# Kernel optimization log

Measured on AMD Instinct MI355X. Metric: run time of the kernel, lower is better.

## Reference

```python
import jax, jax.numpy as jnp
import numpy as np

EPS = 1.1920929e-07  # torch RMSNorm default eps = finfo(fp32).eps


def _rmsnorm(x, w):
    return x * jax.lax.rsqrt(jnp.mean(x * x, axis=-1, keepdims=True) + EPS) * w


def setup_inputs() -> dict:
    B, S, D, H, SD = 2, 2048, 1024, 16, 64
    ks = jax.random.split(jax.random.key(0), 16)
    scale = 0.02
    return {
        "x": jax.random.normal(ks[0], (B, S, D), jnp.float32),
        "gamma": jax.random.normal(ks[1], (1, 1, D), jnp.float32),
        "beta": jax.random.normal(ks[2], (1, 1, D), jnp.float32),
        "state": jax.random.normal(ks[3], (B, SD), jnp.float32),
        # weights stored as (in, out) so y = x @ W
        "w_qkv": jax.random.normal(ks[4], (D, 3 * D), jnp.float32) * scale,
        "w_o": jax.random.normal(ks[5], (D, D), jnp.float32) * scale,
        "w_gate": jax.random.normal(ks[6], (D, 3 * D), jnp.float32) * scale,
        "w_up": jax.random.normal(ks[7], (D, 3 * D), jnp.float32) * scale,
        "w_down": jax.random.normal(ks[8], (3 * D, D), jnp.float32) * scale,
        "norm1_w": jnp.ones((D,), jnp.float32),
        "norm2_w": jnp.ones((D,), jnp.float32),
        "w_state_mod": jax.random.normal(ks[9], (SD, 2 * D), jnp.float32) * scale,
        "w_h2s": jax.random.normal(ks[10], (D, SD), jnp.float32) * scale,
        "w_sgate": jax.random.normal(ks[11], (2 * SD, SD), jnp.float32) * scale,
    }


def reference(x, gamma, beta, state, w_qkv, w_o, w_gate, w_up, w_down,
              norm1_w, norm2_w, w_state_mod, w_h2s, w_sgate):
    B, S, D = x.shape
    H = 16
    hd = D // H

    # state-conditioned FiLM modulation
    state_mod = state @ w_state_mod                      # (B, 2D)
    state_gamma = 1.0 + state_mod[:, :D][:, None, :]     # (B, 1, D)
    state_beta = state_mod[:, D:][:, None, :]
    full_gamma = gamma * state_gamma
    full_beta = beta + state_beta

    # attention branch
    h = _rmsnorm(x, norm1_w) * full_gamma + full_beta
    qkv = (h @ w_qkv).reshape(B, S, 3, H, hd)
    q = qkv[:, :, 0].transpose(0, 2, 1, 3)               # (B, H, S, hd)
    k = qkv[:, :, 1].transpose(0, 2, 1, 3)
    v = qkv[:, :, 2].transpose(0, 2, 1, 3)
    scores = jnp.einsum('bhqd,bhkd->bhqk', q, k) / np.sqrt(hd).astype(np.float32)
    causal = jnp.tril(jnp.ones((S, S), bool))
    scores = jnp.where(causal, scores, -jnp.inf)
    attn = jax.nn.softmax(scores, axis=-1)
    out = jnp.einsum('bhqk,bhkd->bhqd', attn, v).transpose(0, 2, 1, 3).reshape(B, S, D)
    x = x + out @ w_o

    # SwiGLU FFN branch (same FiLM params)
    h2 = _rmsnorm(x, norm2_w) * full_gamma + full_beta
    gate = jax.nn.silu(h2 @ w_gate)
    x = x + (gate * (h2 @ w_up)) @ w_down

    # recurrent state update
    new_info = jnp.mean(x, axis=1) @ w_h2s               # (B, SD)
    update_gate = jax.nn.sigmoid(jnp.concatenate([state, new_info], axis=-1) @ w_sgate)
    new_state = state * (1.0 - update_gate) + new_info * update_gate
    return x, new_state
```

## Files before the change

kernel.cpp:

```cpp
#include <hip/hip_runtime.h>
#include <hip/hip_bf16.h>

#define EPS_RMS 1.1920929e-07f

constexpr int B_ = 2, S_ = 2048, D_ = 1024, H_ = 16, HD_ = 64, SD_ = 64;
constexpr int M_ = B_ * S_;
constexpr int D3_ = 3 * D_;

using short8 = __attribute__((ext_vector_type(8))) short;
using f32x4  = __attribute__((ext_vector_type(4))) float;
using f32x16 = __attribute__((ext_vector_type(16))) float;
typedef int v2i __attribute__((ext_vector_type(2)));

static __device__ __forceinline__ ushort f2bf(float x) {
  __hip_bfloat16 h = __float2bfloat16(x);
  return *reinterpret_cast<ushort*>(&h);
}
static __device__ __forceinline__ float bf2f(ushort u) {
  __hip_bfloat16 h;
  *reinterpret_cast<ushort*>(&h) = u;
  return __bfloat162float(h);
}
static __device__ __forceinline__ unsigned pk2(float lo, float hi) {
  return (unsigned)f2bf(lo) | ((unsigned)f2bf(hi) << 16);
}
static __device__ __forceinline__ v2i swap32(int a, int b) {
  return __builtin_amdgcn_permlane32_swap(a, b, false, false);
}
struct alignas(8) bf4 { ushort a, b, c, d; };

static __device__ __forceinline__ void gload16(const ushort* g, ushort* l) {
  __builtin_amdgcn_global_load_lds(
      (const __attribute__((address_space(1))) unsigned int*)g,
      (__attribute__((address_space(3))) unsigned int*)l, 16, 0, 0);
}

__global__ void film_kernel(const float* __restrict__ state,
                            const float* __restrict__ w_sm,
                            const float* __restrict__ gamma,
                            const float* __restrict__ beta,
                            float* __restrict__ fg, float* __restrict__ fb) {
  int c = blockIdx.x * 256 + threadIdx.x;
  int b = blockIdx.y;
  float acc = 0.f;
#pragma unroll 8
  for (int k = 0; k < SD_; ++k)
    acc += state[b * SD_ + k] * w_sm[k * (2 * D_) + c];
  if (c < D_) fg[b * D_ + c] = gamma[c] * (1.f + acc);
  else        fb[b * D_ + (c - D_)] = beta[c - D_] + acc;
}

__global__ __launch_bounds__(256) void rmsnorm_film_kernel(
    const float* __restrict__ X, const float* __restrict__ nw,
    const float* __restrict__ fg, const float* __restrict__ fb,
    ushort* __restrict__ Hout) {
  int row = blockIdx.x;
  int b = row / S_;
  int t = threadIdx.x;
  const float4* x4 = (const float4*)(X + (size_t)row * D_);
  float4 xv = x4[t];
  float ss = xv.x * xv.x + xv.y * xv.y + xv.z * xv.z + xv.w * xv.w;
#pragma unroll
  for (int off = 32; off >= 1; off >>= 1) ss += __shfl_xor(ss, off);
  __shared__ float red[4];
  if ((t & 63) == 0) red[t >> 6] = ss;
  __syncthreads();
  float tot = red[0] + red[1] + red[2] + red[3];
  float scale = rsqrtf(tot / (float)D_ + EPS_RMS);
  int d = t * 4;
  const float4 nw4 = *(const float4*)(nw + d);
  const float4 g4  = *(const float4*)(fg + b * D_ + d);
  const float4 b4  = *(const float4*)(fb + b * D_ + d);
  bf4 hv;
  hv.a = f2bf(xv.x * scale * nw4.x * g4.x + b4.x);
  hv.b = f2bf(xv.y * scale * nw4.y * g4.y + b4.y);
  hv.c = f2bf(xv.z * scale * nw4.z * g4.z + b4.z);
  hv.d = f2bf(xv.w * scale * nw4.w * g4.w + b4.w);
  *(bf4*)(Hout + (size_t)row * D_ + d) = hv;
}

__global__ __launch_bounds__(256) void transpose_bf16(
    const float* __restrict__ W, ushort* __restrict__ Wt, int K, int N) {
  __shared__ float tile[32][33];
  int n0 = blockIdx.x * 32, k0 = blockIdx.y * 32;
  int t = threadIdx.x;
  int c = t & 31, r = t >> 5;
#pragma unroll
  for (int p = 0; p < 4; ++p)
    tile[r + 8 * p][c] = W[(size_t)(k0 + r + 8 * p) * N + n0 + c];
  __syncthreads();
#pragma unroll
  for (int p = 0; p < 4; ++p)
    Wt[(size_t)(n0 + r + 8 * p) * K + k0 + c] = f2bf(tile[c][r + 8 * p]);
}

__global__ __launch_bounds__(256) void transpose_bf16_dual(
    const float* __restrict__ W0, ushort* __restrict__ T0,
    const float* __restrict__ W1, ushort* __restrict__ T1, int K, int N) {
  const float* W = blockIdx.z ? W1 : W0;
  ushort* Wt = blockIdx.z ? T1 : T0;
  __shared__ float tile[32][33];
  int n0 = blockIdx.x * 32, k0 = blockIdx.y * 32;
  int t = threadIdx.x;
  int c = t & 31, r = t >> 5;
#pragma unroll
  for (int p = 0; p < 4; ++p)
    tile[r + 8 * p][c] = W[(size_t)(k0 + r + 8 * p) * N + n0 + c];
  __syncthreads();
#pragma unroll
  for (int p = 0; p < 4; ++p)
    Wt[(size_t)(n0 + r + 8 * p) * K + k0 + c] = f2bf(tile[c][r + 8 * p]);
}

static __device__ __forceinline__ void mfma_tile(
    const char* Au, const char* Bu, f32x4 (&acc)[4][4],
    int l15, int l4, int swz, int wr, int wc) {
#pragma unroll
  for (int kk = 0; kk < 2; ++kk) {
    int tslot = ((kk * 4 + l4) ^ swz) << 4;
    short8 a[4], b[4];
#pragma unroll
    for (int i = 0; i < 4; ++i) {
      int arow = wr * 64 + i * 16 + l15;
      int brow = wc * 64 + i * 16 + l15;
      a[i] = *(const short8*)(Au + arow * 128 + tslot);
      b[i] = *(const short8*)(Bu + brow * 128 + tslot);
    }
#pragma unroll
    for (int m = 0; m < 4; ++m)
#pragma unroll
      for (int n = 0; n < 4; ++n)
        acc[m][n] = __builtin_amdgcn_mfma_f32_16x16x32_bf16(a[m], b[n], acc[m][n], 0, 0, 0);
  }
}

static __device__ __forceinline__ void block_swizzle(int bid, int M, int N,
                                                     int& bm, int& bn) {
  int nbn = N >> 7;
  int nb  = nbn * (M >> 7);
  int qx  = nb >> 3;
  int lin = (bid & 7) * qx + (bid >> 3);
  int grp = lin / (nbn << 3), rem = lin % (nbn << 3);
  bm = ((grp << 3) + (rem & 7)) << 7;
  bn = (rem >> 3) << 7;
}

template<int EPI>
__global__ __launch_bounds__(256, 3) void gemm_mfma(
    const ushort* __restrict__ A, const ushort* __restrict__ Bt,
    const float* __restrict__ Res,
    float* __restrict__ Cf, ushort* __restrict__ Cb, ushort* __restrict__ VtP,
    int M, int N, int K) {
  __shared__ ushort smem[16384];
  char* Au = (char*)smem;
  char* Bu = (char*)(smem + 8192);
  int t = threadIdx.x;
  int bm, bn;
  block_swizzle(blockIdx.x, M, N, bm, bn);

  int lane = t & 63, wid = t >> 6;
  int wr = wid >> 1, wc = wid & 1;
  int l15 = lane & 15, l4 = lane >> 4;
  int swz = l15 & 7;

  const ushort* gA[4];
  const ushort* gB[4];
  ushort* lA[4];
  ushort* lB[4];
#pragma unroll
  for (int p = 0; p < 4; ++p) {
    int seg = p * 4 + wid;
    int flat = seg * 64 + lane;
    int row = flat >> 3, sl = flat & 7;
    int gc = ((sl ^ (row & 7)) << 3);
    gA[p] = A  + (size_t)(bm + row) * K + gc;
    gB[p] = Bt + (size_t)(bn + row) * K + gc;
    lA[p] = smem + seg * 512;
    lB[p] = smem + 8192 + seg * 512;
  }

  f32x4 acc[4][4];
#pragma unroll
  for (int m = 0; m < 4; ++m)
#pragma unroll
    for (int n = 0; n < 4; ++n) acc[m][n] = (f32x4){0.f, 0.f, 0.f, 0.f};

  int nk = K >> 6;
  for (int kt = 0; kt < nk; ++kt) {
    __syncthreads();
#pragma unroll
    for (int p = 0; p < 4; ++p) {
      gload16(gA[p], lA[p]);
      gload16(gB[p], lB[p]);
      gA[p] += 64; gB[p] += 64;
    }
    __syncthreads();
    mfma_tile(Au, Bu, acc, l15, l4, swz, wr, wc);
  }

  if constexpr (EPI == 3) {
#pragma unroll
    for (int m = 0; m < 4; ++m)
#pragma unroll
      for (int n = 0; n < 4; ++n) {
        int row0 = bm + wr * 64 + m * 16 + l4 * 4;
        int col  = bn + wc * 64 + n * 16 + l15;
#pragma unroll
        for (int j = 0; j < 4; ++j) {
          size_t idx = (size_t)(row0 + j) * (size_t)N + col;
          Cf[idx] = Res[idx] + acc[m][n][j];
        }
      }
  } else {
    __syncthreads();
    ushort* Es = smem;
    bool vblk = (bn >= 2048);
#pragma unroll
    for (int m = 0; m < 4; ++m)
#pragma unroll
      for (int n = 0; n < 4; ++n) {
        int rb0 = wr * 64 + m * 16 + l4 * 4;
        int c   = wc * 64 + n * 16 + l15;
#pragma unroll
        for (int j = 0; j < 4; ++j) {
          float v = acc[m][n][j];
          int r = rb0 + j;
          if (vblk) Es[c * 128 + (r ^ ((c & 15) << 3))] = f2bf(v);
          else      Es[r * 128 + c] = f2bf(v);
        }
      }
    __syncthreads();
    if (vblk) {
#pragma unroll
      for (int p = 0; p < 8; ++p) {
        int flat = p * 256 + t;
        int c = flat >> 4, r8 = (flat & 15) * 8;
        int vc = bn - 2048 + c, hh = vc >> 6, dd = vc & 63;
        int bbv = bm >> 11, s0 = (bm & 2047) + r8;
        *(short8*)(VtP + ((((size_t)bbv * 16 + hh) * 64 + dd) << 11) + s0) =
            *(const short8*)&Es[c * 128 + (r8 ^ ((c & 15) << 3))];
      }
    } else {
#pragma unroll
      for (int p = 0; p < 8; ++p) {
        int flat = p * 256 + t;
        int r = flat >> 4, c8 = (flat & 15) * 8;
        *(short8*)(Cb + (size_t)(bm + r) * N + bn + c8) = *(const short8*)&Es[r * 128 + c8];
      }
    }
  }
}

__global__ __launch_bounds__(256, 2) void gemm_dual(
    const ushort* __restrict__ A, const ushort* __restrict__ Gt,
    const ushort* __restrict__ Ut, ushort* __restrict__ Cb,
    int M, int N, int K) {
  __shared__ ushort smem[24576];
  char* Au = (char*)smem;
  char* Gu = (char*)(smem + 8192);
  char* Uu = (char*)(smem + 16384);
  int t = threadIdx.x;
  int bm, bn;
  block_swizzle(blockIdx.x, M, N, bm, bn);

  int lane = t & 63, wid = t >> 6;
  int wr = wid >> 1, wc = wid & 1;
  int l15 = lane & 15, l4 = lane >> 4;
  int swz = l15 & 7;

  const ushort* gA[4]; const ushort* gG[4]; const ushort* gU[4];
  ushort* lA[4]; ushort* lG[4]; ushort* lU[4];
#pragma unroll
  for (int p = 0; p < 4; ++p) {
    int seg = p * 4 + wid;
    int flat = seg * 64 + lane;
    int row = flat >> 3, sl = flat & 7;
    int gc = ((sl ^ (row & 7)) << 3);
    gA[p] = A  + (size_t)(bm + row) * K + gc;
    gG[p] = Gt + (size_t)(bn + row) * K + gc;
    gU[p] = Ut + (size_t)(bn + row) * K + gc;
    lA[p] = smem + seg * 512;
    lG[p] = smem + 8192 + seg * 512;
    lU[p] = smem + 16384 + seg * 512;
  }

  f32x4 ag[4][4], au[4][4];
#pragma unroll
  for (int m = 0; m < 4; ++m)
#pragma unroll
    for (int n = 0; n < 4; ++n) {
      ag[m][n] = (f32x4){0.f, 0.f, 0.f, 0.f};
      au[m][n] = (f32x4){0.f, 0.f, 0.f, 0.f};
    }

  int nk = K >> 6;
  for (int kt = 0; kt < nk; ++kt) {
    __syncthreads();
#pragma unroll
    for (int p = 0; p < 4; ++p) {
      gload16(gA[p], lA[p]);
      gload16(gG[p], lG[p]);
      gload16(gU[p], lU[p]);
      gA[p] += 64; gG[p] += 64; gU[p] += 64;
    }
    __syncthreads();
#pragma unroll
    for (int kk = 0; kk < 2; ++kk) {
      int tslot = ((kk * 4 + l4) ^ swz) << 4;
      short8 a[4], bg[4], bu[4];
#pragma unroll
      for (int i = 0; i < 4; ++i) {
        int arow = wr * 64 + i * 16 + l15;
        int brow = wc * 64 + i * 16 + l15;
        a[i]  = *(const short8*)(Au + arow * 128 + tslot);
        bg[i] = *(const short8*)(Gu + brow * 128 + tslot);
        bu[i] = *(const short8*)(Uu + brow * 128 + tslot);
      }
#pragma unroll
      for (int m = 0; m < 4; ++m)
#pragma unroll
        for (int n = 0; n < 4; ++n) {
          ag[m][n] = __builtin_amdgcn_mfma_f32_16x16x32_bf16(a[m], bg[n], ag[m][n], 0, 0, 0);
          au[m][n] = __builtin_amdgcn_mfma_f32_16x16x32_bf16(a[m], bu[n], au[m][n], 0, 0, 0);
        }
    }
  }

  __syncthreads();
  ushort* Es = smem;
#pragma unroll
  for (int m = 0; m < 4; ++m)
#pragma unroll
    for (int n = 0; n < 4; ++n) {
      int rb0 = wr * 64 + m * 16 + l4 * 4;
      int c   = wc * 64 + n * 16 + l15;
#pragma unroll
      for (int j = 0; j < 4; ++j) {
        float gv = ag[m][n][j];
        float v = gv / (1.f + __expf(-gv)) * au[m][n][j];
        Es[(rb0 + j) * 128 + c] = f2bf(v);
      }
    }
  __syncthreads();
#pragma unroll
  for (int p = 0; p < 8; ++p) {
    int flat = p * 256 + t;
    int r = flat >> 4, c8 = (flat & 15) * 8;
    *(short8*)(Cb + (size_t)(bm + r) * N + bn + c8) = *(const short8*)&Es[r * 128 + c8];
  }
}

__global__ __launch_bounds__(512, 2) void attn_mfma_kernel(
    const ushort* __restrict__ qkv,
    const ushort* __restrict__ Vt,
    ushort* __restrict__ AO) {
  __shared__ ushort lds[16384];
  const float SL2 = 0.125f * 1.44269504f;
  int t = threadIdx.x;
  int x = blockIdx.x;
  int lin = ((x & 7) << 5) + (x >> 3);
  int pp = lin & 7;
  int hb = lin >> 3;
  int h = hb & 15, bb = hb >> 4;
  int lane = t & 63, wv = t >> 6;
  int qi = wv >> 2, wsub = wv & 3;
  int qt = qi ? (15 - pp) : pp;
  int q0 = qt * 128;
  int l31 = lane & 31, g = lane >> 5;

  int qrow = q0 + wsub * 32 + l31;
  const ushort* qrow_ptr = qkv + (size_t)(bb * S_ + qrow) * 3072 + h * 64;
  short8 qf[4];
#pragma unroll
  for (int s = 0; s < 4; ++s) qf[s] = *(const short8*)(qrow_ptr + s * 16 + g * 8);

  f32x16 accO[2];
#pragma unroll
  for (int u = 0; u < 2; ++u)
#pragma unroll
    for (int r = 0; r < 16; ++r) accO[u][r] = 0.f;
  float m = -INFINITY, l = 0.f;
  int qg = qrow;
  int qmin = q0 + wsub * 32, qmax = qmin + 31;
  int nt = 2 * (16 - pp);

  const ushort* kbase = qkv + (size_t)(bb * S_) * 3072 + 1024 + h * 64;
  const ushort* vbase = Vt + ((size_t)(bb * 16 + h) * 64) * 2048;

  int srow = t >> 3, sslot = t & 7;
  int soff = srow * 64 + ((sslot ^ (srow & 7)) << 3);
  const ushort* kg0 = kbase + (size_t)srow * 3072 + sslot * 8;
  const ushort* vg0 = vbase + (size_t)srow * 2048 + sslot * 8;

  *(short8*)&lds[soff] = *(const short8*)kg0;
  *(short8*)&lds[4096 + soff] = *(const short8*)vg0;
  __syncthreads();

  for (int kti = 0; kti < nt; ++kti) {
    int cur = kti & 1;
    int kt = kti << 6;
    bool pf = (kti + 1 < nt);
    short8 rk, rv;
    if (pf) {
      rk = *(const short8*)(kg0 + (size_t)(kti + 1) * (64 * 3072));
      rv = *(const short8*)(vg0 + (kti + 1) * 64);
    }
    if (kt <= qmax) {
      const ushort* Kb = lds + cur * 8192;
      const ushort* Vb = Kb + 4096;

      f32x16 accT[2];
#pragma unroll
      for (int t2 = 0; t2 < 2; ++t2)
#pragma unroll
        for (int r = 0; r < 16; ++r) accT[t2][r] = 0.f;
      __builtin_amdgcn_s_setprio(1);
#pragma unroll
      for (int t2 = 0; t2 < 2; ++t2) {
        int key = 32 * t2 + l31;
#pragma unroll
        for (int s = 0; s < 4; ++s) {
          short8 kf = *(const short8*)&Kb[key * 64 + (((2 * s + g) ^ (key & 7)) << 3)];
          accT[t2] = __builtin_amdgcn_mfma_f32_32x32x16_bf16(kf, qf[s], accT[t2], 0, 0, 0);
        }
      }
      __builtin_amdgcn_s_setprio(0);

      bool need_mask = (kt + 63 > qmin);
      float p_[2][16];
      float pmax = -INFINITY;
#pragma unroll
      for (int t2 = 0; t2 < 2; ++t2)
#pragma unroll
        for (int r = 0; r < 16; ++r) {
          float v = accT[t2][r] * SL2;
          if (need_mask) {
            int key = kt + 32 * t2 + (r & 3) + 8 * (r >> 2) + 4 * g;
            if (key > qg) v = -INFINITY;
          }
          p_[t2][r] = v;
          pmax = fmaxf(pmax, v);
        }
      {
        v2i pm = swap32(__float_as_int(pmax), __float_as_int(pmax));
        pmax = fmaxf(pmax, __int_as_float(g ? pm.x : pm.y));
      }

      if (__any(pmax > m + 11.5f)) {
        float mnew = fmaxf(m, pmax);
        float corr = exp2f(m - mnew);
        m = mnew;
        l *= corr;
        float cr[16];
#pragma unroll
        for (int r = 0; r < 16; ++r) cr[r] = __shfl(corr, (r & 3) + 8 * (r >> 2) + 4 * g);
#pragma unroll
        for (int r = 0; r < 16; ++r) { accO[0][r] *= cr[r]; accO[1][r] *= cr[r]; }
      }
      float psum = 0.f;
#pragma unroll
      for (int t2 = 0; t2 < 2; ++t2)
#pragma unroll
        for (int r = 0; r < 16; ++r) {
          float e = exp2f(p_[t2][r] - m);
          p_[t2][r] = e;
          psum += e;
        }
      {
        v2i ps = swap32(__float_as_int(psum), __float_as_int(psum));
        psum += __int_as_float(g ? ps.x : ps.y);
      }
      l += psum;

#pragma unroll
      for (int s = 0; s < 4; ++s) {
        int ca = 2 * s, cb2 = 2 * s + 1;
        int ta = ca >> 2, ra = (ca & 3) * 4;
        int tb = cb2 >> 2, rbq = (cb2 & 3) * 4;
        int w0a = (int)pk2(p_[ta][ra], p_[ta][ra + 1]);
        int w1a = (int)pk2(p_[ta][ra + 2], p_[ta][ra + 3]);
        int w0b = (int)pk2(p_[tb][rbq], p_[tb][rbq + 1]);
        int w1b = (int)pk2(p_[tb][rbq + 2], p_[tb][rbq + 3]);
        v2i r0 = swap32(w0a, w0b);
        v2i r1 = swap32(w1a, w1b);
        union { int u[4]; short8 s8; } pa;
        pa.u[0] = r0.x;
        pa.u[1] = r1.x;
        pa.u[2] = r0.y;
        pa.u[3] = r1.y;
        __builtin_amdgcn_s_setprio(1);
#pragma unroll
        for (int u = 0; u < 2; ++u) {
          int d = 32 * u + l31;
          short8 vf = *(const short8*)&Vb[d * 64 + (((2 * s + g) ^ (d & 7)) << 3)];
          accO[u] = __builtin_amdgcn_mfma_f32_32x32x16_bf16(pa.s8, vf, accO[u], 0, 0, 0);
        }
        __builtin_amdgcn_s_setprio(0);
      }
    }
    if (pf) {
      ushort* dst = lds + (cur ^ 1) * 8192;
      *(short8*)&dst[soff] = rk;
      *(short8*)&dst[4096 + soff] = rv;
    }
    __syncthreads();
  }

  float linv = 1.f / l;
  float lr[16];
#pragma unroll
  for (int r = 0; r < 16; ++r) lr[r] = __shfl(linv, (r & 3) + 8 * (r >> 2) + 4 * g);
#pragma unroll
  for (int r = 0; r < 16; ++r) {
    int row = wv * 32 + (r & 3) + 8 * (r >> 2) + 4 * g;
    lds[row * 64 + l31]      = f2bf(accO[0][r] * lr[r]);
    lds[row * 64 + 32 + l31] = f2bf(accO[1][r] * lr[r]);
  }
  __syncthreads();
#pragma unroll
  for (int p = 0; p < 4; ++p) {
    int flat = p * 512 + t;
    int row = flat >> 3, slot = flat & 7;
    int qto = (row < 128) ? pp : (15 - pp);
    int grow = row & 127;
    *(short8*)(AO + (size_t)(bb * S_ + qto * 128 + grow) * 1024 + h * 64 + slot * 8) =
        *(const short8*)&lds[row * 64 + slot * 8];
  }
}

__global__ void colmean1(const float* __restrict__ X, float* __restrict__ part) {
  int d = blockIdx.x * 256 + threadIdx.x;
  int b = blockIdx.y;
  int ch = blockIdx.z;
  float s = 0.f;
  int s0 = ch * (S_ / 16);
  for (int i = 0; i < S_ / 16; ++i)
    s += X[(size_t)(b * S_ + s0 + i) * D_ + d];
  part[(b * 16 + ch) * D_ + d] = s;
}
__global__ void colmean2(const float* __restrict__ part, float* __restrict__ cm) {
  int d = blockIdx.x * 256 + threadIdx.x;
  int b = blockIdx.y;
  float s = 0.f;
#pragma unroll
  for (int c = 0; c < 16; ++c) s += part[(b * 16 + c) * D_ + d];
  cm[b * D_ + d] = s * (1.f / (float)S_);
}

__global__ __launch_bounds__(128) void state_kernel(
    const float* __restrict__ cm, const float* __restrict__ state,
    const float* __restrict__ w_h2s, const float* __restrict__ w_sg,
    float* __restrict__ out_tail) {
  int t = threadIdx.x;
  int b = t >> 6, j = t & 63;
  float ni = 0.f;
  for (int k = 0; k < D_; ++k) ni += cm[b * D_ + k] * w_h2s[k * SD_ + j];
  __shared__ float ni_s[128];
  ni_s[t] = ni;
  __syncthreads();
  float g = 0.f;
#pragma unroll
  for (int k = 0; k < SD_; ++k) g += state[b * SD_ + k] * w_sg[k * SD_ + j];
#pragma unroll
  for (int k = 0; k < SD_; ++k) g += ni_s[b * SD_ + k] * w_sg[(SD_ + k) * SD_ + j];
  g = 1.f / (1.f + __expf(-g));
  float st = state[b * SD_ + j];
  out_tail[b * SD_ + j] = st * (1.f - g) + ni * g;
}

extern "C" void kernel_launch(void* const* d_in, const int* in_sizes, int n_in,
                              void* d_out, int out_size, void* d_ws, size_t ws_size,
                              hipStream_t stream) {
  const float* x      = (const float*)d_in[0];
  const float* gamma  = (const float*)d_in[1];
  const float* beta   = (const float*)d_in[2];
  const float* state  = (const float*)d_in[3];
  const float* w_qkv  = (const float*)d_in[4];
  const float* w_o    = (const float*)d_in[5];
  const float* w_gate = (const float*)d_in[6];
  const float* w_up   = (const float*)d_in[7];
  const float* w_down = (const float*)d_in[8];
  const float* norm1w = (const float*)d_in[9];
  const float* norm2w = (const float*)d_in[10];
  const float* w_sm   = (const float*)d_in[11];
  const float* w_h2s  = (const float*)d_in[12];
  const float* w_sg   = (const float*)d_in[13];
  float* out = (float*)d_out;

  float* ws = (float*)d_ws;
  float*  fg     = ws;
  float*  fb     = ws + 2048;
  float*  cm     = ws + 4096;
  float*  part   = ws + 8192;
  ushort* h_bf   = (ushort*)(ws + 65536);
  ushort* AO_bf  = (ushort*)(ws + 65536 + 2097152);
  ushort* wT     = (ushort*)(ws + 65536 + 2 * 2097152);
  ushort* wT2    = (ushort*)(ws + 65536 + 2 * 2097152 + 1572864);
  ushort* qkv_bf = (ushort*)(ws + 65536 + 2 * 2097152 + 2 * 1572864);
  ushort* Vt_g   = (ushort*)(ws + 65536 + 2 * 2097152 + 2 * 1572864 + 6291456);
  ushort* gu_bf  = qkv_bf;

  film_kernel<<<dim3(8, B_), 256, 0, stream>>>(state, w_sm, gamma, beta, fg, fb);
  rmsnorm_film_kernel<<<M_, 256, 0, stream>>>(x, norm1w, fg, fb, h_bf);
  transpose_bf16<<<dim3(D3_ / 32, D_ / 32), 256, 0, stream>>>(w_qkv, wT, D_, D3_);
  gemm_mfma<4><<<(D3_ / 128) * (M_ / 128), 256, 0, stream>>>(
      h_bf, wT, nullptr, nullptr, qkv_bf, Vt_g, M_, D3_, D_);
  attn_mfma_kernel<<<256, 512, 0, stream>>>(qkv_bf, Vt_g, AO_bf);
  transpose_bf16<<<dim3(D_ / 32, D_ / 32), 256, 0, stream>>>(w_o, wT, D_, D_);
  gemm_mfma<3><<<(D_ / 128) * (M_ / 128), 256, 0, stream>>>(
      AO_bf, wT, x, out, nullptr, nullptr, M_, D_, D_);
  rmsnorm_film_kernel<<<M_, 256, 0, stream>>>(out, norm2w, fg, fb, h_bf);
  transpose_bf16_dual<<<dim3(D3_ / 32, D_ / 32, 2), 256, 0, stream>>>(
      w_gate, wT, w_up, wT2, D_, D3_);
  gemm_dual<<<(D3_ / 128) * (M_ / 128), 256, 0, stream>>>(
      h_bf, wT, wT2, gu_bf, M_, D3_, D_);
  transpose_bf16<<<dim3(D_ / 32, D3_ / 32), 256, 0, stream>>>(w_down, wT, D3_, D_);
  gemm_mfma<3><<<(D_ / 128) * (M_ / 128), 256, 0, stream>>>(
      gu_bf, wT, out, out, nullptr, nullptr, M_, D_, D3_);
  colmean1<<<dim3(4, B_, 16), 256, 0, stream>>>(out, part);
  colmean2<<<dim3(4, B_), 256, 0, stream>>>(part, cm);
  state_kernel<<<1, 128, 0, stream>>>(cm, state, w_h2s, w_sg, out + (size_t)M_ * D_);
}
```

Measured before the change: 317.3 us.

## Split attention blocks into one query tile each, longest-first scheduling

The attention kernel previously paired a short and a long causal query tile in one 512-thread block to balance work. It now launches 512 blocks of 256 threads, each handling a single 128-row query tile, ordered so the heaviest tiles are dispatched first, and K/V staging now uses two loads per thread. Launch bounds are adjusted for higher occupancy, and gemm_dual also gets a higher occupancy hint. This trades the paired-tile balancing for finer-grained blocks and dynamic scheduling, which may help latency hiding but loses K/V tile sharing across the two query tiles.

```diff
diff --git a/kernel.cpp b/kernel.cpp
--- a/kernel.cpp
+++ b/kernel.cpp
@@ -251,7 +251,7 @@
   }
 }
 
-__global__ __launch_bounds__(256, 2) void gemm_dual(
+__global__ __launch_bounds__(256, 3) void gemm_dual(
     const ushort* __restrict__ A, const ushort* __restrict__ Gt,
     const ushort* __restrict__ Ut, ushort* __restrict__ Cb,
     int M, int N, int K) {
@@ -350,7 +350,7 @@
   }
 }
 
-__global__ __launch_bounds__(512, 2) void attn_mfma_kernel(
+__global__ __launch_bounds__(256, 4) void attn_mfma_kernel(
     const ushort* __restrict__ qkv,
     const ushort* __restrict__ Vt,
     ushort* __restrict__ AO) {
@@ -358,17 +358,15 @@
   const float SL2 = 0.125f * 1.44269504f;
   int t = threadIdx.x;
   int x = blockIdx.x;
-  int lin = ((x & 7) << 5) + (x >> 3);
-  int pp = lin & 7;
-  int hb = lin >> 3;
+  int lin = ((x & 7) << 6) + (x >> 3);
+  int qt = 15 - (lin & 15);
+  int hb = lin >> 4;
   int h = hb & 15, bb = hb >> 4;
+  int q0 = qt * 128;
   int lane = t & 63, wv = t >> 6;
-  int qi = wv >> 2, wsub = wv & 3;
-  int qt = qi ? (15 - pp) : pp;
-  int q0 = qt * 128;
   int l31 = lane & 31, g = lane >> 5;
 
-  int qrow = q0 + wsub * 32 + l31;
+  int qrow = q0 + wv * 32 + l31;
   const ushort* qrow_ptr = qkv + (size_t)(bb * S_ + qrow) * 3072 + h * 64;
   short8 qf[4];
 #pragma unroll
@@ -381,29 +379,42 @@
     for (int r = 0; r < 16; ++r) accO[u][r] = 0.f;
   float m = -INFINITY, l = 0.f;
   int qg = qrow;
-  int qmin = q0 + wsub * 32, qmax = qmin + 31;
-  int nt = 2 * (16 - pp);
+  int qmin = q0 + wv * 32, qmax = qmin + 31;
+  int nt = 2 * qt + 2;
 
   const ushort* kbase = qkv + (size_t)(bb * S_) * 3072 + 1024 + h * 64;
   const ushort* vbase = Vt + ((size_t)(bb * 16 + h) * 64) * 2048;
 
-  int srow = t >> 3, sslot = t & 7;
-  int soff = srow * 64 + ((sslot ^ (srow & 7)) << 3);
-  const ushort* kg0 = kbase + (size_t)srow * 3072 + sslot * 8;
-  const ushort* vg0 = vbase + (size_t)srow * 2048 + sslot * 8;
-
-  *(short8*)&lds[soff] = *(const short8*)kg0;
-  *(short8*)&lds[4096 + soff] = *(const short8*)vg0;
+  int soff[2];
+  const ushort* kg0[2];
+  const ushort* vg0[2];
+#pragma unroll
+  for (int p = 0; p < 2; ++p) {
+    int flat = p * 256 + t;
+    int row = flat >> 3, sl = flat & 7;
+    soff[p] = row * 64 + ((sl ^ (row & 7)) << 3);
+    kg0[p] = kbase + (size_t)row * 3072 + sl * 8;
+    vg0[p] = vbase + (size_t)row * 2048 + sl * 8;
+  }
+
+#pragma unroll
+  for (int p = 0; p < 2; ++p) {
+    *(short8*)&lds[soff[p]] = *(const short8*)kg0[p];
+    *(short8*)&lds[4096 + soff[p]] = *(const short8*)vg0[p];
+  }
   __syncthreads();
 
   for (int kti = 0; kti < nt; ++kti) {
     int cur = kti & 1;
     int kt = kti << 6;
     bool pf = (kti + 1 < nt);
-    short8 rk, rv;
+    short8 rk[2], rv[2];
     if (pf) {
-      rk = *(const short8*)(kg0 + (size_t)(kti + 1) * (64 * 3072));
-      rv = *(const short8*)(vg0 + (kti + 1) * 64);
+#pragma unroll
+      for (int p = 0; p < 2; ++p) {
+        rk[p] = *(const short8*)(kg0[p] + (size_t)(kti + 1) * (64 * 3072));
+        rv[p] = *(const short8*)(vg0[p] + (kti + 1) * 64);
+      }
     }
     if (kt <= qmax) {
       const ushort* Kb = lds + cur * 8192;
@@ -500,8 +511,11 @@
     }
     if (pf) {
       ushort* dst = lds + (cur ^ 1) * 8192;
-      *(short8*)&dst[soff] = rk;
-      *(short8*)&dst[4096 + soff] = rv;
+#pragma unroll
+      for (int p = 0; p < 2; ++p) {
+        *(short8*)&dst[soff[p]] = rk[p];
+        *(short8*)&dst[4096 + soff[p]] = rv[p];
+      }
     }
     __syncthreads();
   }
@@ -519,11 +533,9 @@
   __syncthreads();
 #pragma unroll
   for (int p = 0; p < 4; ++p) {
-    int flat = p * 512 + t;
+    int flat = p * 256 + t;
     int row = flat >> 3, slot = flat & 7;
-    int qto = (row < 128) ? pp : (15 - pp);
-    int grow = row & 127;
-    *(short8*)(AO + (size_t)(bb * S_ + qto * 128 + grow) * 1024 + h * 64 + slot * 8) =
+    *(short8*)(AO + (size_t)(bb * S_ + q0 + row) * 1024 + h * 64 + slot * 8) =
         *(const short8*)&lds[row * 64 + slot * 8];
   }
 }
@@ -605,7 +617,7 @@
   transpose_bf16<<<dim3(D3_ / 32, D_ / 32), 256, 0, stream>>>(w_qkv, wT, D_, D3_);
   gemm_mfma<4><<<(D3_ / 128) * (M_ / 128), 256, 0, stream>>>(
       h_bf, wT, nullptr, nullptr, qkv_bf, Vt_g, M_, D3_, D_);
-  attn_mfma_kernel<<<256, 512, 0, stream>>>(qkv_bf, Vt_g, AO_bf);
+  attn_mfma_kernel<<<512, 256, 0, stream>>>(qkv_bf, Vt_g, AO_bf);
   transpose_bf16<<<dim3(D_ / 32, D_ / 32), 256, 0, stream>>>(w_o, wT, D_, D_);
   gemm_mfma<3><<<(D_ / 128) * (M_ / 128), 256, 0, stream>>>(
       AO_bf, wT, x, out, nullptr, nullptr, M_, D_, D_);
```

Result: slower. 382.2 us (+20.5%).
